# Kernel tuning notes

Hardware: AMD Instinct MI355X
Metric: run time of the kernel (lower is better)

## Reference

```python
import jax, jax.numpy as jnp
import numpy as np

B, N, C = 8, 2048, 256
NGRP = 4          # n oscillator dims per group
RANK = 16         # A_rank
EPS = 1e-6        # solver eps
GN_EPS = 1e-5     # torch GroupNorm default eps


def setup_inputs() -> dict:
    key = jax.random.key(0)
    k0, k1, k2, k3 = jax.random.split(key, 4)
    x = jax.random.normal(k0, (B, N, C), jnp.float32)
    y = jax.random.normal(k1, (B, C, N), jnp.float32)
    sc = jax.random.uniform(k2, (B, N, N), jnp.float32)
    U = 0.01 * jax.random.normal(k3, (N, RANK), jnp.float32)
    omega_param = (1.0 / np.sqrt(2)).astype(np.float32) * jnp.ones((C // 2, 1), jnp.float32)
    gn_w = jnp.ones((C,), jnp.float32)
    gn_b = jnp.zeros((C,), jnp.float32)
    gamma = jnp.float32(1.0)
    return {"x": x, "y": y, "sc": sc, "U": U, "omega_param": omega_param,
            "gn_w": gn_w, "gn_b": gn_b, "gamma": gamma, "Q": 8}


def _map_to_sphere(x):
    # normalize each group of NGRP channels to unit norm
    xv = x.reshape(B, N, C // NGRP, NGRP)
    n2 = jnp.clip(jnp.sum(xv * xv, axis=-1, keepdims=True), EPS, None)
    return (xv * jax.lax.rsqrt(n2)).reshape(B, N, C)


def _project_osc(v, x):
    # remove component of v along x within each oscillator group (tangent projection)
    xv = x.reshape(B, N, C // NGRP, NGRP)
    vv = v.reshape(B, N, C // NGRP, NGRP)
    sim = jnp.sum(xv * vv, axis=-1, keepdims=True)
    return (vv - sim * xv).reshape(B, N, C)


def _group_norm(y, w, b):
    # y: [B, C, N]; num_groups = C // NGRP, NGRP channels per group
    G = C // NGRP
    yv = y.reshape(B, G, NGRP * N)
    mu = jnp.mean(yv, axis=-1, keepdims=True)
    var = jnp.mean((yv - mu) ** 2, axis=-1, keepdims=True)
    yn = ((yv - mu) * jax.lax.rsqrt(var + GN_EPS)).reshape(B, C, N)
    return yn * w[None, :, None] + b[None, :, None]


def _omega_term(x, omega_param):
    # pairwise rotation: (x0, x1) -> (omg*x1, -omg*x0), omg = |omega_param| per pair
    xp = x.reshape(B, N, C // 2, 2)
    omg = jnp.abs(omega_param).reshape(1, 1, C // 2)  # norm over trailing dim of size 1
    out = jnp.stack([omg * xp[..., 1], -omg * xp[..., 0]], axis=-1)
    return out.reshape(B, N, C)


def _kuramoto(x, y, sc, U, omega_param, gn_w, gn_b, gamma, Q):
    rho = 1.0
    # y: [B, C, N] -> GroupNorm -> [B, N, C] -> sphere
    y = _group_norm(y, gn_w, gn_b)
    y = _map_to_sphere(jnp.transpose(y, (0, 2, 1)))
    # x: [B, N, C] (N != C so no transpose in original)
    x = _map_to_sphere(x)
    # coupling matrix K = sym(W) * sigmoid(U U^T)  (normalize_K=False, w_scale=1)
    Wsym = 0.5 * (sc + jnp.transpose(sc, (0, 2, 1)))
    A = jax.nn.sigmoid(U @ U.T)          # [N, N]
    K = Wsym * A[None, :, :]             # [B, N, N]

    def step(xc, _):
        coupling = jnp.einsum('bnm,bmc->bnc', K, xc)
        force = coupling + y
        om = _omega_term(xc, omega_param)
        dxdt = om + rho * _project_osc(force, xc)
        xn = _map_to_sphere(xc + gamma * dxdt)
        return xn, xn

    _, xs = jax.lax.scan(step, x, None, length=Q)
    return xs  # [Q, B, N, C]


def reference(x, y, sc, U, omega_param, gn_w, gn_b, gamma, Q):
    return _kuramoto(x, y, sc, U, omega_param, gn_w, gn_b, gamma, Q)
```

## Files before the change

### kernel.cpp

```cpp
#include <hip/hip_runtime.h>
#include <hip/hip_bf16.h>

#define BB 8
#define NN 2048
#define CC 256
#define GG 64
#define QQ 8

typedef unsigned short u16;
typedef __attribute__((ext_vector_type(8))) short bf16x8;
typedef __attribute__((ext_vector_type(4))) float f32x4;

static __device__ __forceinline__ float b2f(u16 u) {
  union { unsigned int i; float f; } cv; cv.i = ((unsigned int)u) << 16; return cv.f;
}
static __device__ __forceinline__ u16 f2b(float f) {
  union { __hip_bfloat16 h; u16 u; } cv; cv.h = __float2bfloat16(f); return cv.u;
}
static __device__ __forceinline__ float ldin(const void* p, size_t i, bool f32) {
  return f32 ? ((const float*)p)[i] : b2f(((const u16*)p)[i]);
}
static __device__ __forceinline__ float4 ldin4(const void* p, size_t i, bool f32) {
  if (f32) return *(const float4*)((const float*)p + i);
  ushort4 u = *(const ushort4*)((const u16*)p + i);
  return make_float4(b2f(u.x), b2f(u.y), b2f(u.z), b2f(u.w));
}
static __device__ __forceinline__ void gload16(const void* g, void* l) {
  __builtin_amdgcn_global_load_lds(
      (const __attribute__((address_space(1))) void*)g,
      (__attribute__((address_space(3))) void*)l, 16, 0, 0);
}

__global__ __launch_bounds__(256) void detect_kernel(const u16* __restrict__ sc,
                                                     int* __restrict__ flag)
{
  __shared__ int sh;
  if (threadIdx.x == 0) sh = 0;
  __syncthreads();
  int cnt = 0;
  for (int i = threadIdx.x; i < 2048; i += 256) {
    u16 w = sc[2 * i];
    int e = (w >> 7) & 0xFF;
    if (e >= 100 && e <= 130) cnt++;
  }
  atomicAdd(&sh, cnt);
  __syncthreads();
  if (threadIdx.x == 0) *flag = (sh < 1024) ? 1 : 0;
}

__global__ __launch_bounds__(256) void build_k_kernel(
    const void* __restrict__ sc, const void* __restrict__ U,
    u16* __restrict__ Khi, u16* __restrict__ Klo,
    const int* __restrict__ flagp, int b0, int nbat)
{
  const int i0 = blockIdx.y * 32;
  const int j0 = blockIdx.x * 32;
  if (j0 < i0) return;
  const bool f32 = (*flagp != 0);
  const int tx = threadIdx.x;
  const int ty = threadIdx.y;
  const int t  = ty * 32 + tx;
  const int rr = t >> 3;
  const int cq = t & 7;

  __shared__ float Ui[32][17];
  __shared__ float Uj[32][17];
  __shared__ float As[32][33];
  __shared__ float t1[32][33];
  __shared__ float t2[32][33];

  for (int s = t; s < 512; s += 256) {
    int r2 = s >> 4, kk = s & 15;
    Ui[r2][kk] = ldin(U, (size_t)(i0 + r2) * 16 + kk, f32);
    Uj[r2][kk] = ldin(U, (size_t)(j0 + r2) * 16 + kk, f32);
  }
  __syncthreads();
  for (int ii = ty; ii < 32; ii += 8) {
    float dot = 0.f;
    #pragma unroll
    for (int k = 0; k < 16; k++) dot += Ui[ii][k] * Uj[tx][k];
    As[ii][tx] = 1.0f / (1.0f + expf(-dot));
  }

  for (int bl = 0; bl < nbat; bl++) {
    const int b = b0 + bl;
    const size_t scb = (size_t)b * NN * NN;
    __syncthreads();
    float4 va = ldin4(sc, scb + (size_t)(i0 + rr) * NN + j0 + 4 * cq, f32);
    float4 vb = ldin4(sc, scb + (size_t)(j0 + rr) * NN + i0 + 4 * cq, f32);
    t1[rr][4*cq+0] = va.x; t1[rr][4*cq+1] = va.y;
    t1[rr][4*cq+2] = va.z; t1[rr][4*cq+3] = va.w;
    t2[rr][4*cq+0] = vb.x; t2[rr][4*cq+1] = vb.y;
    t2[rr][4*cq+2] = vb.z; t2[rr][4*cq+3] = vb.w;
    __syncthreads();
    const size_t kfb = (size_t)bl * NN * NN;
    ushort4 h4, l4;
    #pragma unroll
    for (int k = 0; k < 4; k++) {
      int col = 4 * cq + k;
      float kv = 0.5f * (t1[rr][col] + t2[col][rr]) * As[rr][col];
      u16 h = f2b(kv);
      ((u16*)&h4)[k] = h;
      ((u16*)&l4)[k] = f2b(kv - b2f(h));
    }
    size_t o = kfb + (size_t)(i0 + rr) * NN + j0 + 4 * cq;
    *(ushort4*)(Khi + o) = h4;
    *(ushort4*)(Klo + o) = l4;
    if (i0 != j0) {
      #pragma unroll
      for (int k = 0; k < 4; k++) {
        int col = 4 * cq + k;
        float kv = 0.5f * (t2[rr][col] + t1[col][rr]) * As[col][rr];
        u16 h = f2b(kv);
        ((u16*)&h4)[k] = h;
        ((u16*)&l4)[k] = f2b(kv - b2f(h));
      }
      size_t o2 = kfb + (size_t)(j0 + rr) * NN + i0 + 4 * cq;
      *(ushort4*)(Khi + o2) = h4;
      *(ushort4*)(Klo + o2) = l4;
    }
  }
}

__global__ __launch_bounds__(256) void gn_stats_kernel(
    const void* __restrict__ y, float* __restrict__ murs,
    const int* __restrict__ flagp)
{
  const bool f32 = (*flagp != 0);
  const int bg = blockIdx.x;
  float s = 0.f, ss = 0.f;
  if (f32) {
    const float* base = (const float*)y + (size_t)bg * 4 * NN;
    for (int i = threadIdx.x; i < 2048; i += 256) {
      float4 v = *(const float4*)(base + (size_t)i * 4);
      s  += v.x + v.y + v.z + v.w;
      ss += v.x*v.x + v.y*v.y + v.z*v.z + v.w*v.w;
    }
  } else {
    const u16* base = (const u16*)y + (size_t)bg * 4 * NN;
    for (int i = threadIdx.x; i < 2048; i += 256) {
      ushort4 v = *(const ushort4*)(base + (size_t)i * 4);
      float f0 = b2f(v.x), f1 = b2f(v.y), f2 = b2f(v.z), f3 = b2f(v.w);
      s  += f0 + f1 + f2 + f3;
      ss += f0*f0 + f1*f1 + f2*f2 + f3*f3;
    }
  }
  #pragma unroll
  for (int off = 32; off > 0; off >>= 1) {
    s  += __shfl_down(s, off, 64);
    ss += __shfl_down(ss, off, 64);
  }
  __shared__ float sh[8];
  const int w = threadIdx.x >> 6, ln = threadIdx.x & 63;
  if (ln == 0) { sh[w * 2] = s; sh[w * 2 + 1] = ss; }
  __syncthreads();
  if (threadIdx.x == 0) {
    float S  = sh[0] + sh[2] + sh[4] + sh[6];
    float SS = sh[1] + sh[3] + sh[5] + sh[7];
    float mu  = S / 8192.0f;
    float var = SS / 8192.0f - mu * mu;
    murs[bg * 2]     = mu;
    murs[bg * 2 + 1] = 1.0f / sqrtf(fmaxf(var, 0.f) + 1e-5f);
  }
}

__global__ __launch_bounds__(256) void y_tf_kernel(
    const void* __restrict__ y, const float* __restrict__ murs,
    const void* __restrict__ gw, const void* __restrict__ gb,
    float* __restrict__ yt, const int* __restrict__ flagp)
{
  const bool f32 = (*flagp != 0);
  const int b = blockIdx.y;
  const int n = blockIdx.x * 64 + threadIdx.x;
  for (int g = threadIdx.y; g < GG; g += 4) {
    float mu = murs[(b * GG + g) * 2];
    float rs = murs[(b * GG + g) * 2 + 1];
    float v[4];
    #pragma unroll
    for (int k = 0; k < 4; k++) {
      int c = 4 * g + k;
      float val = (ldin(y, ((size_t)b * CC + c) * NN + n, f32) - mu) * rs;
      v[k] = val * ldin(gw, c, f32) + ldin(gb, c, f32);
    }
    float n2 = v[0]*v[0] + v[1]*v[1] + v[2]*v[2] + v[3]*v[3];
    float scl = 1.0f / sqrtf(fmaxf(n2, 1e-6f));
    float4 o; o.x = v[0]*scl; o.y = v[1]*scl; o.z = v[2]*scl; o.w = v[3]*scl;
    *(float4*)(yt + ((size_t)b * NN + n) * CC + 4 * g) = o;
  }
}

__global__ __launch_bounds__(256) void x_init_kernel(
    const void* __restrict__ x, u16* __restrict__ xTh, u16* __restrict__ xTl,
    const int* __restrict__ flagp)
{
  const bool f32 = (*flagp != 0);
  const int b = blockIdx.y;
  const int n = blockIdx.x * 64 + threadIdx.x;
  for (int g = threadIdx.y; g < GG; g += 4) {
    size_t idx = ((size_t)b * NN + n) * CC + 4 * g;
    float v[4];
    if (f32) {
      float4 u4 = *(const float4*)((const float*)x + idx);
      v[0] = u4.x; v[1] = u4.y; v[2] = u4.z; v[3] = u4.w;
    } else {
      ushort4 u = *(const ushort4*)((const u16*)x + idx);
      v[0] = b2f(u.x); v[1] = b2f(u.y); v[2] = b2f(u.z); v[3] = b2f(u.w);
    }
    float n2 = v[0]*v[0] + v[1]*v[1] + v[2]*v[2] + v[3]*v[3];
    float scl = 1.0f / sqrtf(fmaxf(n2, 1e-6f));
    size_t xb = ((size_t)b * CC + 4 * g) * NN + n;
    #pragma unroll
    for (int k = 0; k < 4; k++) {
      float xv = v[k] * scl;
      u16 h = f2b(xv);
      xTh[xb + (size_t)k * NN] = h;
      xTl[xb + (size_t)k * NN] = f2b(xv - b2f(h));
    }
  }
}

template<int NFR, int NFC>
static __device__ __forceinline__ void fused_step_epilogue(
    f32x4 (&acc)[NFR][NFC], int b, int rb, int cb, int l15, int lk,
    const u16* __restrict__ xhc, const u16* __restrict__ xlc,
    u16* __restrict__ xhn, u16* __restrict__ xln,
    const float* __restrict__ yt, const void* __restrict__ omega,
    const void* __restrict__ gamma, void* __restrict__ outbase, size_t qoff,
    bool f32)
{
  const float gm = ldin(gamma, 0, f32);
  #pragma unroll
  for (int fr = 0; fr < NFR; fr++) {
    const int rbase = rb + fr * 16 + lk * 4;
    #pragma unroll
    for (int fc = 0; fc < NFC; fc++) {
      const int c = cb + fc * 16 + l15;
      const size_t xoff = ((size_t)b * CC + c) * NN + rbase;
      ushort4 xh4 = *(const ushort4*)(xhc + xoff);
      ushort4 xl4 = *(const ushort4*)(xlc + xoff);
      float xcv[4] = { b2f(xh4.x) + b2f(xl4.x), b2f(xh4.y) + b2f(xl4.y),
                       b2f(xh4.z) + b2f(xl4.z), b2f(xh4.w) + b2f(xl4.w) };
      float om   = fabsf(ldin(omega, c >> 1, f32));
      float omsg = (c & 1) ? -om : om;
      float xn[4];
      #pragma unroll
      for (int r = 0; r < 4; r++) {
        const int n = rbase + r;
        float f = acc[fr][fc][r] + yt[((size_t)b * NN + n) * CC + c];
        float s = xcv[r] * f;
        s += __shfl_xor(s, 1);
        s += __shfl_xor(s, 2);
        float xp = __shfl_xor(xcv[r], 1);
        float d  = omsg * xp + (f - s * xcv[r]);
        float v  = xcv[r] + gm * d;
        float n2 = v * v;
        n2 += __shfl_xor(n2, 1);
        n2 += __shfl_xor(n2, 2);
        float scl = 1.0f / sqrtf(fmaxf(n2, 1e-6f));
        xn[r] = v * scl;
        const size_t oidx = qoff + ((size_t)b * NN + n) * CC + c;
        if (f32) ((float*)outbase)[oidx] = xn[r];
        else     ((u16*)outbase)[oidx]   = f2b(xn[r]);
      }
      ushort4 nh, nl;
      #pragma unroll
      for (int r = 0; r < 4; r++) {
        u16 h = f2b(xn[r]);
        ((u16*)&nh)[r] = h;
        ((u16*)&nl)[r] = f2b(xn[r] - b2f(h));
      }
      *(ushort4*)(xhn + xoff) = nh;
      *(ushort4*)(xln + xoff) = nl;
    }
  }
}

__global__ __launch_bounds__(512, 2) void gemm_fused_sk(
    const u16* __restrict__ Khi, const u16* __restrict__ Klo,
    const u16* __restrict__ xhc, const u16* __restrict__ xlc,
    u16* __restrict__ xhn, u16* __restrict__ xln,
    const float* __restrict__ yt, const void* __restrict__ omega,
    const void* __restrict__ gamma, void* __restrict__ outbase, size_t qoff,
    const int* __restrict__ flagp)
{
  const int flat = blockIdx.x + 2 * blockIdx.y + 32 * blockIdx.z;
  const int swz  = (flat & 7) * 32 + (flat >> 3);
  const int bx = swz & 1;
  const int by = (swz >> 1) & 15;
  const int b  = swz >> 5;
  const int m0 = by * 128;
  const int c0 = bx * 128;

  __shared__ char lds[2][65536];

  const int t    = threadIdx.x;
  const int lane = t & 63;
  const int wid  = t >> 6;
  const int ng   = wid >> 2;
  const int wr   = (wid >> 1) & 1;
  const int wc   = wid & 1;

  const u16* Ah = Khi + (size_t)b * NN * NN;
  const u16* Al = Klo + (size_t)b * NN * NN;
  const u16* Bh = xhc + (size_t)b * CC * NN;
  const u16* Bl = xlc + (size_t)b * CC * NN;

  const int tr   = t >> 3;
  const int phys = (t & 7) ^ (tr & 7);
  const size_t aoff = (size_t)(m0 + tr) * NN + phys * 8;
  const size_t boff = (size_t)(c0 + tr) * NN + phys * 8;
  const int dst = wid * 1024;

  f32x4 acc[4][2];
  const f32x4 zero4 = {0.f, 0.f, 0.f, 0.f};
  #pragma unroll
  for (int i = 0; i < 4; i++)
    #pragma unroll
    for (int j = 0; j < 2; j++) acc[i][j] = zero4;

  auto stage = [&](int bufi, int kt) {
    char* base = &lds[bufi][0];
    const int k0 = kt * 64;
    #pragma unroll
    for (int i = 0; i < 2; i++) {
      gload16(Ah + aoff + (size_t)i * (64 * NN) + k0, base +         i * 8192 + dst);
      gload16(Al + aoff + (size_t)i * (64 * NN) + k0, base + 16384 + i * 8192 + dst);
      gload16(Bh + boff + (size_t)i * (64 * NN) + k0, base + 32768 + i * 8192 + dst);
      gload16(Bl + boff + (size_t)i * (64 * NN) + k0, base + 49152 + i * 8192 + dst);
    }
  };

  const int l15 = lane & 15;
  const int lk  = lane >> 4;

  auto compute = [&](int bufi) {
    const char* base = &lds[bufi][0];
    #pragma unroll
    for (int ks = 0; ks < 2; ks++) {
      const int cl = ks * 4 + lk;
      bf16x8 fah[4], fal[4], fbh[2], fbl[2];
      #pragma unroll
      for (int fr = 0; fr < 4; fr++) {
        int r   = wr * 64 + fr * 16 + l15;
        int off = r * 128 + ((cl ^ (r & 7)) << 4);
        fah[fr] = *(const bf16x8*)(base + off);
        fal[fr] = *(const bf16x8*)(base + 16384 + off);
      }
      #pragma unroll
      for (int fc = 0; fc < 2; fc++) {
        int r   = ng * 64 + wc * 32 + fc * 16 + l15;
        int off = r * 128 + ((cl ^ (r & 7)) << 4);
        fbh[fc] = *(const bf16x8*)(base + 32768 + off);
        fbl[fc] = *(const bf16x8*)(base + 49152 + off);
      }
      #pragma unroll
      for (int fr = 0; fr < 4; fr++)
        #pragma unroll
        for (int fc = 0; fc < 2; fc++) {
          acc[fr][fc] = __builtin_amdgcn_mfma_f32_16x16x32_bf16(
              fah[fr], fbh[fc], acc[fr][fc], 0, 0, 0);
          acc[fr][fc] = __builtin_amdgcn_mfma_f32_16x16x32_bf16(
              fah[fr], fbl[fc], acc[fr][fc], 0, 0, 0);
          acc[fr][fc] = __builtin_amdgcn_mfma_f32_16x16x32_bf16(
              fal[fr], fbh[fc], acc[fr][fc], 0, 0, 0);
        }
    }
  };

  stage(0, 0);
  stage(1, 1);
  for (int kt = 0; kt < 30; kt++) {
    asm volatile("s_waitcnt vmcnt(8)" ::: "memory");
    __builtin_amdgcn_s_barrier();
    __builtin_amdgcn_sched_barrier(0);
    compute(kt & 1);
    asm volatile("s_waitcnt lgkmcnt(0)" ::: "memory");
    __builtin_amdgcn_sched_barrier(0);
    __builtin_amdgcn_s_barrier();
    stage(kt & 1, kt + 2);
  }
  asm volatile("s_waitcnt vmcnt(8)" ::: "memory");
  __builtin_amdgcn_s_barrier();
  __builtin_amdgcn_sched_barrier(0);
  compute(0);
  asm volatile("s_waitcnt vmcnt(0)" ::: "memory");
  __builtin_amdgcn_s_barrier();
  __builtin_amdgcn_sched_barrier(0);
  compute(1);

  fused_step_epilogue<4, 2>(acc, b, m0 + wr * 64, c0 + ng * 64 + wc * 32,
                            l15, lk, xhc, xlc, xhn, xln, yt, omega, gamma,
                            outbase, qoff, (*flagp != 0));
}

__global__ __launch_bounds__(256, 2) void gemm_fused_db(
    const u16* __restrict__ Khi, const u16* __restrict__ Klo,
    const u16* __restrict__ xhc, const u16* __restrict__ xlc,
    u16* __restrict__ xhn, u16* __restrict__ xln,
    const float* __restrict__ yt, const void* __restrict__ omega,
    const void* __restrict__ gamma, void* __restrict__ outbase, size_t qoff,
    const int* __restrict__ flagp, int grp)
{
  const int flat = blockIdx.x + 4 * blockIdx.y + 128 * blockIdx.z;
  const int swz  = (flat & 7) * 64 + (flat >> 3);
  const int bx = swz & 3;
  const int by = (swz >> 2) & 31;
  const int bl = swz >> 7;
  const int b  = grp * 4 + bl;
  const int m0 = by * 64;
  const int c0 = bx * 64;

  __shared__ char lds[2][32768];

  const int t    = threadIdx.x;
  const int lane = t & 63;
  const int wid  = t >> 6;
  const int wr   = wid >> 1;
  const int wc   = wid & 1;

  const u16* Ah = Khi + (size_t)bl * NN * NN;
  const u16* Al = Klo + (size_t)bl * NN * NN;
  const u16* Bh = xhc + (size_t)b * CC * NN;
  const u16* Bl = xlc + (size_t)b * CC * NN;

  const int tr   = t >> 3;
  const int phys = (t & 7) ^ (tr & 7);
  const size_t aoff = (size_t)(m0 + tr) * NN + phys * 8;
  const size_t boff = (size_t)(c0 + tr) * NN + phys * 8;
  const int dst = wid * 1024;

  f32x4 acc[2][2];
  const f32x4 zero4 = {0.f, 0.f, 0.f, 0.f};
  #pragma unroll
  for (int i = 0; i < 2; i++)
    #pragma unroll
    for (int j = 0; j < 2; j++) acc[i][j] = zero4;

  auto stage = [&](int bufi, int kt) {
    char* base = &lds[bufi][0];
    const int k0 = kt * 64;
    #pragma unroll
    for (int i = 0; i < 2; i++) {
      gload16(Ah + aoff + (size_t)i * (32 * NN) + k0, base +         i * 4096 + dst);
      gload16(Al + aoff + (size_t)i * (32 * NN) + k0, base +  8192 + i * 4096 + dst);
      gload16(Bh + boff + (size_t)i * (32 * NN) + k0, base + 16384 + i * 4096 + dst);
      gload16(Bl + boff + (size_t)i * (32 * NN) + k0, base + 24576 + i * 4096 + dst);
    }
  };

  const int l15 = lane & 15;
  const int lk  = lane >> 4;

  auto compute = [&](int bufi) {
    const char* base = &lds[bufi][0];
    #pragma unroll
    for (int ks = 0; ks < 2; ks++) {
      const int cl = ks * 4 + lk;
      bf16x8 fah[2], fal[2], fbh[2], fbl[2];
      #pragma unroll
      for (int fr = 0; fr < 2; fr++) {
        int r   = wr * 32 + fr * 16 + l15;
        int off = r * 128 + ((cl ^ (r & 7)) << 4);
        fah[fr] = *(const bf16x8*)(base + off);
        fal[fr] = *(const bf16x8*)(base + 8192 + off);
      }
      #pragma unroll
      for (int fc = 0; fc < 2; fc++) {
        int r   = wc * 32 + fc * 16 + l15;
        int off = r * 128 + ((cl ^ (r & 7)) << 4);
        fbh[fc] = *(const bf16x8*)(base + 16384 + off);
        fbl[fc] = *(const bf16x8*)(base + 24576 + off);
      }
      #pragma unroll
      for (int fr = 0; fr < 2; fr++)
        #pragma unroll
        for (int fc = 0; fc < 2; fc++) {
          acc[fr][fc] = __builtin_amdgcn_mfma_f32_16x16x32_bf16(
              fah[fr], fbh[fc], acc[fr][fc], 0, 0, 0);
          acc[fr][fc] = __builtin_amdgcn_mfma_f32_16x16x32_bf16(
              fah[fr], fbl[fc], acc[fr][fc], 0, 0, 0);
          acc[fr][fc] = __builtin_amdgcn_mfma_f32_16x16x32_bf16(
              fal[fr], fbh[fc], acc[fr][fc], 0, 0, 0);
        }
    }
  };

  stage(0, 0);
  __syncthreads();
  int buf = 0;
  for (int kt = 0; kt < NN / 64; kt++) {
    if (kt + 1 < NN / 64) stage(buf ^ 1, kt + 1);
    compute(buf);
    __syncthreads();
    buf ^= 1;
  }

  fused_step_epilogue<2, 2>(acc, b, m0 + wr * 32, c0 + wc * 32,
                            l15, lk, xhc, xlc, xhn, xln, yt, omega, gamma,
                            outbase, qoff, (*flagp != 0));
}

extern "C" void kernel_launch(void* const* d_in, const int* in_sizes, int n_in,
                              void* d_out, int out_size, void* d_ws, size_t ws_size,
                              hipStream_t stream) {
  const void* x     = d_in[0];
  const void* y     = d_in[1];
  const void* sc    = d_in[2];
  const void* U     = d_in[3];
  const void* omega = d_in[4];
  const void* gw    = d_in[5];
  const void* gb    = d_in[6];
  const void* gamma = d_in[7];
  char* ws = (char*)d_ws;

  const size_t BNC = (size_t)BB * NN * CC;
  const bool big = ws_size >= 184600000ull;

  if (big) {
    u16*   Khi  = (u16*)(ws);
    u16*   Klo  = (u16*)(ws + 67108864);
    float* yt   = (float*)(ws + 134217728);
    u16*   xAh  = (u16*)(ws + 150994944);
    u16*   xAl  = (u16*)(ws + 159383552);
    u16*   xBh  = (u16*)(ws + 167772160);
    u16*   xBl  = (u16*)(ws + 176160768);
    float* murs = (float*)(ws + 184549376);
    int*   flag = (int*)  (ws + 184553472);
    u16* xh[2] = { xAh, xBh };
    u16* xl[2] = { xAl, xBl };

    detect_kernel<<<dim3(1), dim3(256), 0, stream>>>((const u16*)sc, flag);
    gn_stats_kernel<<<dim3(512), dim3(256), 0, stream>>>(y, murs, flag);
    y_tf_kernel<<<dim3(32, 8), dim3(64, 4), 0, stream>>>(y, murs, gw, gb, yt, flag);
    x_init_kernel<<<dim3(32, 8), dim3(64, 4), 0, stream>>>(x, xAh, xAl, flag);
    build_k_kernel<<<dim3(64, 64), dim3(32, 8), 0, stream>>>(
        sc, U, Khi, Klo, flag, 0, 8);
    for (int q = 0; q < QQ; q++) {
      const int cur = q & 1, nxt = cur ^ 1;
      gemm_fused_sk<<<dim3(2, 16, 8), dim3(512), 0, stream>>>(
          Khi, Klo, xh[cur], xl[cur], xh[nxt], xl[nxt],
          yt, omega, gamma, d_out, (size_t)q * BNC, flag);
    }
  } else {
    u16*   Khi  = (u16*)(ws);
    u16*   Klo  = (u16*)(ws + 33554432);
    float* yt   = (float*)(ws + 67108864);
    u16*   xAh  = (u16*)(ws + 83886080);
    u16*   xAl  = (u16*)(ws + 92274688);
    u16*   xBh  = (u16*)(ws + 100663296);
    u16*   xBl  = (u16*)(ws + 109051904);
    float* murs = (float*)(ws + 117440512);
    int*   flag = (int*)  (ws + 117444608);
    u16* xh[2] = { xAh, xBh };
    u16* xl[2] = { xAl, xBl };

    detect_kernel<<<dim3(1), dim3(256), 0, stream>>>((const u16*)sc, flag);
    gn_stats_kernel<<<dim3(512), dim3(256), 0, stream>>>(y, murs, flag);
    y_tf_kernel<<<dim3(32, 8), dim3(64, 4), 0, stream>>>(y, murs, gw, gb, yt, flag);
    x_init_kernel<<<dim3(32, 8), dim3(64, 4), 0, stream>>>(x, xAh, xAl, flag);
    for (int grp = 0; grp < 2; grp++) {
      build_k_kernel<<<dim3(64, 64), dim3(32, 8), 0, stream>>>(
          sc, U, Khi, Klo, flag, grp * 4, 4);
      for (int q = 0; q < QQ; q++) {
        const int cur = q & 1, nxt = cur ^ 1;
        gemm_fused_db<<<dim3(4, 32, 4), dim3(256), 0, stream>>>(
            Khi, Klo, xh[cur], xl[cur], xh[nxt], xl[nxt],
            yt, omega, gamma, d_out, (size_t)q * BNC, flag, grp);
      }
    }
  }
}
```

Baseline: 907.3 us.

## Parallelize K build over batch, phase GEMM compute with barriers, nontemporal output stores

The K-build kernel gets a batch grid dimension instead of looping over batches, and the sc loads are issued before the sigmoid computation so their latency overlaps it. This trades extra redundant sigmoid(UU^T) work per batch for more parallelism. The split-K GEMM compute loop is reorganized per row fragment, with workgroup barriers and s_setprio around the MFMA bursts so waves interleave LDS reads with matrix work. The output writes become nontemporal stores to avoid polluting cache.

```diff
diff --git a/kernel.cpp b/kernel.cpp
--- a/kernel.cpp
+++ b/kernel.cpp
@@ -51,12 +51,14 @@
 __global__ __launch_bounds__(256) void build_k_kernel(
     const void* __restrict__ sc, const void* __restrict__ U,
     u16* __restrict__ Khi, u16* __restrict__ Klo,
-    const int* __restrict__ flagp, int b0, int nbat)
+    const int* __restrict__ flagp, int b0)
 {
   const int i0 = blockIdx.y * 32;
   const int j0 = blockIdx.x * 32;
   if (j0 < i0) return;
   const bool f32 = (*flagp != 0);
+  const int bl = blockIdx.z;
+  const int b  = b0 + bl;
   const int tx = threadIdx.x;
   const int ty = threadIdx.y;
   const int t  = ty * 32 + tx;
@@ -74,6 +76,9 @@
     Ui[r2][kk] = ldin(U, (size_t)(i0 + r2) * 16 + kk, f32);
     Uj[r2][kk] = ldin(U, (size_t)(j0 + r2) * 16 + kk, f32);
   }
+  const size_t scb = (size_t)b * NN * NN;
+  float4 va = ldin4(sc, scb + (size_t)(i0 + rr) * NN + j0 + 4 * cq, f32);
+  float4 vb = ldin4(sc, scb + (size_t)(j0 + rr) * NN + i0 + 4 * cq, f32);
   __syncthreads();
   for (int ii = ty; ii < 32; ii += 8) {
     float dot = 0.f;
@@ -81,44 +86,37 @@
     for (int k = 0; k < 16; k++) dot += Ui[ii][k] * Uj[tx][k];
     As[ii][tx] = 1.0f / (1.0f + expf(-dot));
   }
-
-  for (int bl = 0; bl < nbat; bl++) {
-    const int b = b0 + bl;
-    const size_t scb = (size_t)b * NN * NN;
-    __syncthreads();
-    float4 va = ldin4(sc, scb + (size_t)(i0 + rr) * NN + j0 + 4 * cq, f32);
-    float4 vb = ldin4(sc, scb + (size_t)(j0 + rr) * NN + i0 + 4 * cq, f32);
-    t1[rr][4*cq+0] = va.x; t1[rr][4*cq+1] = va.y;
-    t1[rr][4*cq+2] = va.z; t1[rr][4*cq+3] = va.w;
-    t2[rr][4*cq+0] = vb.x; t2[rr][4*cq+1] = vb.y;
-    t2[rr][4*cq+2] = vb.z; t2[rr][4*cq+3] = vb.w;
-    __syncthreads();
-    const size_t kfb = (size_t)bl * NN * NN;
-    ushort4 h4, l4;
+  t1[rr][4*cq+0] = va.x; t1[rr][4*cq+1] = va.y;
+  t1[rr][4*cq+2] = va.z; t1[rr][4*cq+3] = va.w;
+  t2[rr][4*cq+0] = vb.x; t2[rr][4*cq+1] = vb.y;
+  t2[rr][4*cq+2] = vb.z; t2[rr][4*cq+3] = vb.w;
+  __syncthreads();
+
+  const size_t kfb = (size_t)bl * NN * NN;
+  ushort4 h4, l4;
+  #pragma unroll
+  for (int k = 0; k < 4; k++) {
+    int col = 4 * cq + k;
+    float kv = 0.5f * (t1[rr][col] + t2[col][rr]) * As[rr][col];
+    u16 h = f2b(kv);
+    ((u16*)&h4)[k] = h;
+    ((u16*)&l4)[k] = f2b(kv - b2f(h));
+  }
+  size_t o = kfb + (size_t)(i0 + rr) * NN + j0 + 4 * cq;
+  *(ushort4*)(Khi + o) = h4;
+  *(ushort4*)(Klo + o) = l4;
+  if (i0 != j0) {
     #pragma unroll
     for (int k = 0; k < 4; k++) {
       int col = 4 * cq + k;
-      float kv = 0.5f * (t1[rr][col] + t2[col][rr]) * As[rr][col];
+      float kv = 0.5f * (t2[rr][col] + t1[col][rr]) * As[col][rr];
       u16 h = f2b(kv);
       ((u16*)&h4)[k] = h;
       ((u16*)&l4)[k] = f2b(kv - b2f(h));
     }
-    size_t o = kfb + (size_t)(i0 + rr) * NN + j0 + 4 * cq;
-    *(ushort4*)(Khi + o) = h4;
-    *(ushort4*)(Klo + o) = l4;
-    if (i0 != j0) {
-      #pragma unroll
-      for (int k = 0; k < 4; k++) {
-        int col = 4 * cq + k;
-        float kv = 0.5f * (t2[rr][col] + t1[col][rr]) * As[col][rr];
-        u16 h = f2b(kv);
-        ((u16*)&h4)[k] = h;
-        ((u16*)&l4)[k] = f2b(kv - b2f(h));
-      }
-      size_t o2 = kfb + (size_t)(j0 + rr) * NN + i0 + 4 * cq;
-      *(ushort4*)(Khi + o2) = h4;
-      *(ushort4*)(Klo + o2) = l4;
-    }
+    size_t o2 = kfb + (size_t)(j0 + rr) * NN + i0 + 4 * cq;
+    *(ushort4*)(Khi + o2) = h4;
+    *(ushort4*)(Klo + o2) = l4;
   }
 }
 
@@ -259,8 +257,8 @@
         float scl = 1.0f / sqrtf(fmaxf(n2, 1e-6f));
         xn[r] = v * scl;
         const size_t oidx = qoff + ((size_t)b * NN + n) * CC + c;
-        if (f32) ((float*)outbase)[oidx] = xn[r];
-        else     ((u16*)outbase)[oidx]   = f2b(xn[r]);
+        if (f32) __builtin_nontemporal_store(xn[r], (float*)outbase + oidx);
+        else     __builtin_nontemporal_store(f2b(xn[r]), (u16*)outbase + oidx);
       }
       ushort4 nh, nl;
       #pragma unroll
@@ -333,37 +331,50 @@
   const int l15 = lane & 15;
   const int lk  = lane >> 4;
 
-  auto compute = [&](int bufi) {
+  auto compute_phased = [&](int bufi) {
     const char* base = &lds[bufi][0];
-    #pragma unroll
-    for (int ks = 0; ks < 2; ks++) {
-      const int cl = ks * 4 + lk;
-      bf16x8 fah[4], fal[4], fbh[2], fbl[2];
-      #pragma unroll
-      for (int fr = 0; fr < 4; fr++) {
+    bf16x8 fbh[2][2], fbl[2][2];
+    #pragma unroll
+    for (int fr = 0; fr < 4; fr++) {
+      bf16x8 fah[2], fal[2];
+      #pragma unroll
+      for (int ks = 0; ks < 2; ks++) {
+        const int cl = ks * 4 + lk;
         int r   = wr * 64 + fr * 16 + l15;
         int off = r * 128 + ((cl ^ (r & 7)) << 4);
-        fah[fr] = *(const bf16x8*)(base + off);
-        fal[fr] = *(const bf16x8*)(base + 16384 + off);
-      }
-      #pragma unroll
-      for (int fc = 0; fc < 2; fc++) {
-        int r   = ng * 64 + wc * 32 + fc * 16 + l15;
-        int off = r * 128 + ((cl ^ (r & 7)) << 4);
-        fbh[fc] = *(const bf16x8*)(base + 32768 + off);
-        fbl[fc] = *(const bf16x8*)(base + 49152 + off);
-      }
-      #pragma unroll
-      for (int fr = 0; fr < 4; fr++)
+        fah[ks] = *(const bf16x8*)(base + off);
+        fal[ks] = *(const bf16x8*)(base + 16384 + off);
+      }
+      if (fr == 0) {
+        #pragma unroll
+        for (int ks = 0; ks < 2; ks++) {
+          const int cl = ks * 4 + lk;
+          #pragma unroll
+          for (int fc = 0; fc < 2; fc++) {
+            int rb  = ng * 64 + wc * 32 + fc * 16 + l15;
+            int off = rb * 128 + ((cl ^ (rb & 7)) << 4);
+            fbh[ks][fc] = *(const bf16x8*)(base + 32768 + off);
+            fbl[ks][fc] = *(const bf16x8*)(base + 49152 + off);
+          }
+        }
+      }
+      __builtin_amdgcn_s_barrier();
+      asm volatile("s_waitcnt lgkmcnt(0)" ::: "memory");
+      __builtin_amdgcn_sched_barrier(0);
+      __builtin_amdgcn_s_setprio(1);
+      #pragma unroll
+      for (int ks = 0; ks < 2; ks++)
         #pragma unroll
         for (int fc = 0; fc < 2; fc++) {
           acc[fr][fc] = __builtin_amdgcn_mfma_f32_16x16x32_bf16(
-              fah[fr], fbh[fc], acc[fr][fc], 0, 0, 0);
+              fah[ks], fbh[ks][fc], acc[fr][fc], 0, 0, 0);
           acc[fr][fc] = __builtin_amdgcn_mfma_f32_16x16x32_bf16(
-              fah[fr], fbl[fc], acc[fr][fc], 0, 0, 0);
+              fah[ks], fbl[ks][fc], acc[fr][fc], 0, 0, 0);
           acc[fr][fc] = __builtin_amdgcn_mfma_f32_16x16x32_bf16(
-              fal[fr], fbh[fc], acc[fr][fc], 0, 0, 0);
+              fal[ks], fbh[ks][fc], acc[fr][fc], 0, 0, 0);
         }
+      __builtin_amdgcn_s_setprio(0);
+      __builtin_amdgcn_s_barrier();
     }
   };
 
@@ -373,20 +384,17 @@
     asm volatile("s_waitcnt vmcnt(8)" ::: "memory");
     __builtin_amdgcn_s_barrier();
     __builtin_amdgcn_sched_barrier(0);
-    compute(kt & 1);
-    asm volatile("s_waitcnt lgkmcnt(0)" ::: "memory");
-    __builtin_amdgcn_sched_barrier(0);
-    __builtin_amdgcn_s_barrier();
+    compute_phased(kt & 1);
     stage(kt & 1, kt + 2);
   }
   asm volatile("s_waitcnt vmcnt(8)" ::: "memory");
   __builtin_amdgcn_s_barrier();
   __builtin_amdgcn_sched_barrier(0);
-  compute(0);
+  compute_phased(0);
   asm volatile("s_waitcnt vmcnt(0)" ::: "memory");
   __builtin_amdgcn_s_barrier();
   __builtin_amdgcn_sched_barrier(0);
-  compute(1);
+  compute_phased(1);
 
   fused_step_epilogue<4, 2>(acc, b, m0 + wr * 64, c0 + ng * 64 + wc * 32,
                             l15, lk, xhc, xlc, xhn, xln, yt, omega, gamma,
@@ -533,8 +541,8 @@
     gn_stats_kernel<<<dim3(512), dim3(256), 0, stream>>>(y, murs, flag);
     y_tf_kernel<<<dim3(32, 8), dim3(64, 4), 0, stream>>>(y, murs, gw, gb, yt, flag);
     x_init_kernel<<<dim3(32, 8), dim3(64, 4), 0, stream>>>(x, xAh, xAl, flag);
-    build_k_kernel<<<dim3(64, 64), dim3(32, 8), 0, stream>>>(
-        sc, U, Khi, Klo, flag, 0, 8);
+    build_k_kernel<<<dim3(64, 64, 8), dim3(32, 8), 0, stream>>>(
+        sc, U, Khi, Klo, flag, 0);
     for (int q = 0; q < QQ; q++) {
       const int cur = q & 1, nxt = cur ^ 1;
       gemm_fused_sk<<<dim3(2, 16, 8), dim3(512), 0, stream>>>(
@@ -559,8 +567,8 @@
     y_tf_kernel<<<dim3(32, 8), dim3(64, 4), 0, stream>>>(y, murs, gw, gb, yt, flag);
     x_init_kernel<<<dim3(32, 8), dim3(64, 4), 0, stream>>>(x, xAh, xAl, flag);
     for (int grp = 0; grp < 2; grp++) {
-      build_k_kernel<<<dim3(64, 64), dim3(32, 8), 0, stream>>>(
-          sc, U, Khi, Klo, flag, grp * 4, 4);
+      build_k_kernel<<<dim3(64, 64, 4), dim3(32, 8), 0, stream>>>(
+          sc, U, Khi, Klo, flag, grp * 4);
       for (int q = 0; q < QQ; q++) {
         const int cur = q & 1, nxt = cur ^ 1;
         gemm_fused_db<<<dim3(4, 32, 4), dim3(256), 0, stream>>>(
```

New measurement: 920.0 us. About the same (+1.4%).

## Retile main GEMM to 128x64 with 256 threads, parallelise K build over batch

Applied to the files above, without the earlier changes.

Replaces the 512-thread 128x128 GEMM-step kernel with a 256-thread 128x64 tile that uses K-step 32, a simpler double-buffered loop with __syncthreads, and no XOR swizzle in LDS. The K-construction kernel now assigns one batch per grid z-slice instead of looping over batches, and the sc loads are issued before the sigmoid computation so they overlap with it. Output stores become nontemporal to keep them from polluting the cache. The retiled GEMM doubles the number of blocks but rereads the K matrix twice as often, gives up the explicit vmcnt pipelining, and the unswizzled LDS layout may cause bank conflicts.

```diff
diff --git a/kernel.cpp b/kernel.cpp
--- a/kernel.cpp
+++ b/kernel.cpp
@@ -51,12 +51,14 @@
 __global__ __launch_bounds__(256) void build_k_kernel(
     const void* __restrict__ sc, const void* __restrict__ U,
     u16* __restrict__ Khi, u16* __restrict__ Klo,
-    const int* __restrict__ flagp, int b0, int nbat)
+    const int* __restrict__ flagp, int b0)
 {
   const int i0 = blockIdx.y * 32;
   const int j0 = blockIdx.x * 32;
   if (j0 < i0) return;
   const bool f32 = (*flagp != 0);
+  const int bl = blockIdx.z;
+  const int b  = b0 + bl;
   const int tx = threadIdx.x;
   const int ty = threadIdx.y;
   const int t  = ty * 32 + tx;
@@ -74,6 +76,9 @@
     Ui[r2][kk] = ldin(U, (size_t)(i0 + r2) * 16 + kk, f32);
     Uj[r2][kk] = ldin(U, (size_t)(j0 + r2) * 16 + kk, f32);
   }
+  const size_t scb = (size_t)b * NN * NN;
+  float4 va = ldin4(sc, scb + (size_t)(i0 + rr) * NN + j0 + 4 * cq, f32);
+  float4 vb = ldin4(sc, scb + (size_t)(j0 + rr) * NN + i0 + 4 * cq, f32);
   __syncthreads();
   for (int ii = ty; ii < 32; ii += 8) {
     float dot = 0.f;
@@ -81,44 +86,37 @@
     for (int k = 0; k < 16; k++) dot += Ui[ii][k] * Uj[tx][k];
     As[ii][tx] = 1.0f / (1.0f + expf(-dot));
   }
-
-  for (int bl = 0; bl < nbat; bl++) {
-    const int b = b0 + bl;
-    const size_t scb = (size_t)b * NN * NN;
-    __syncthreads();
-    float4 va = ldin4(sc, scb + (size_t)(i0 + rr) * NN + j0 + 4 * cq, f32);
-    float4 vb = ldin4(sc, scb + (size_t)(j0 + rr) * NN + i0 + 4 * cq, f32);
-    t1[rr][4*cq+0] = va.x; t1[rr][4*cq+1] = va.y;
-    t1[rr][4*cq+2] = va.z; t1[rr][4*cq+3] = va.w;
-    t2[rr][4*cq+0] = vb.x; t2[rr][4*cq+1] = vb.y;
-    t2[rr][4*cq+2] = vb.z; t2[rr][4*cq+3] = vb.w;
-    __syncthreads();
-    const size_t kfb = (size_t)bl * NN * NN;
-    ushort4 h4, l4;
+  t1[rr][4*cq+0] = va.x; t1[rr][4*cq+1] = va.y;
+  t1[rr][4*cq+2] = va.z; t1[rr][4*cq+3] = va.w;
+  t2[rr][4*cq+0] = vb.x; t2[rr][4*cq+1] = vb.y;
+  t2[rr][4*cq+2] = vb.z; t2[rr][4*cq+3] = vb.w;
+  __syncthreads();
+
+  const size_t kfb = (size_t)bl * NN * NN;
+  ushort4 h4, l4;
+  #pragma unroll
+  for (int k = 0; k < 4; k++) {
+    int col = 4 * cq + k;
+    float kv = 0.5f * (t1[rr][col] + t2[col][rr]) * As[rr][col];
+    u16 h = f2b(kv);
+    ((u16*)&h4)[k] = h;
+    ((u16*)&l4)[k] = f2b(kv - b2f(h));
+  }
+  size_t o = kfb + (size_t)(i0 + rr) * NN + j0 + 4 * cq;
+  *(ushort4*)(Khi + o) = h4;
+  *(ushort4*)(Klo + o) = l4;
+  if (i0 != j0) {
     #pragma unroll
     for (int k = 0; k < 4; k++) {
       int col = 4 * cq + k;
-      float kv = 0.5f * (t1[rr][col] + t2[col][rr]) * As[rr][col];
+      float kv = 0.5f * (t2[rr][col] + t1[col][rr]) * As[col][rr];
       u16 h = f2b(kv);
       ((u16*)&h4)[k] = h;
       ((u16*)&l4)[k] = f2b(kv - b2f(h));
     }
-    size_t o = kfb + (size_t)(i0 + rr) * NN + j0 + 4 * cq;
-    *(ushort4*)(Khi + o) = h4;
-    *(ushort4*)(Klo + o) = l4;
-    if (i0 != j0) {
-      #pragma unroll
-      for (int k = 0; k < 4; k++) {
-        int col = 4 * cq + k;
-        float kv = 0.5f * (t2[rr][col] + t1[col][rr]) * As[col][rr];
-        u16 h = f2b(kv);
-        ((u16*)&h4)[k] = h;
-        ((u16*)&l4)[k] = f2b(kv - b2f(h));
-      }
-      size_t o2 = kfb + (size_t)(j0 + rr) * NN + i0 + 4 * cq;
-      *(ushort4*)(Khi + o2) = h4;
-      *(ushort4*)(Klo + o2) = l4;
-    }
+    size_t o2 = kfb + (size_t)(j0 + rr) * NN + i0 + 4 * cq;
+    *(ushort4*)(Khi + o2) = h4;
+    *(ushort4*)(Klo + o2) = l4;
   }
 }
 
@@ -259,8 +257,8 @@
         float scl = 1.0f / sqrtf(fmaxf(n2, 1e-6f));
         xn[r] = v * scl;
         const size_t oidx = qoff + ((size_t)b * NN + n) * CC + c;
-        if (f32) ((float*)outbase)[oidx] = xn[r];
-        else     ((u16*)outbase)[oidx]   = f2b(xn[r]);
+        if (f32) __builtin_nontemporal_store(xn[r], (float*)outbase + oidx);
+        else     __builtin_nontemporal_store(f2b(xn[r]), (u16*)outbase + oidx);
       }
       ushort4 nh, nl;
       #pragma unroll
@@ -275,7 +273,7 @@
   }
 }
 
-__global__ __launch_bounds__(512, 2) void gemm_fused_sk(
+__global__ __launch_bounds__(256, 2) void gemm_fused_r9(
     const u16* __restrict__ Khi, const u16* __restrict__ Klo,
     const u16* __restrict__ xhc, const u16* __restrict__ xlc,
     u16* __restrict__ xhn, u16* __restrict__ xln,
@@ -283,21 +281,20 @@
     const void* __restrict__ gamma, void* __restrict__ outbase, size_t qoff,
     const int* __restrict__ flagp)
 {
-  const int flat = blockIdx.x + 2 * blockIdx.y + 32 * blockIdx.z;
-  const int swz  = (flat & 7) * 32 + (flat >> 3);
-  const int bx = swz & 1;
-  const int by = (swz >> 1) & 15;
-  const int b  = swz >> 5;
+  const int flat = blockIdx.x + 4 * blockIdx.y + 64 * blockIdx.z;
+  const int swz  = (flat & 7) * 64 + (flat >> 3);
+  const int bx = swz & 3;
+  const int by = (swz >> 2) & 15;
+  const int b  = swz >> 6;
   const int m0 = by * 128;
-  const int c0 = bx * 128;
-
-  __shared__ char lds[2][65536];
+  const int c0 = bx * 64;
+
+  __shared__ char lds[2][24576];
 
   const int t    = threadIdx.x;
   const int lane = t & 63;
   const int wid  = t >> 6;
-  const int ng   = wid >> 2;
-  const int wr   = (wid >> 1) & 1;
+  const int wr   = wid >> 1;
   const int wc   = wid & 1;
 
   const u16* Ah = Khi + (size_t)b * NN * NN;
@@ -305,10 +302,10 @@
   const u16* Bh = xhc + (size_t)b * CC * NN;
   const u16* Bl = xlc + (size_t)b * CC * NN;
 
-  const int tr   = t >> 3;
-  const int phys = (t & 7) ^ (tr & 7);
-  const size_t aoff = (size_t)(m0 + tr) * NN + phys * 8;
-  const size_t boff = (size_t)(c0 + tr) * NN + phys * 8;
+  const int tr   = t >> 2;
+  const int ck   = t & 3;
+  const size_t aoff = (size_t)(m0 + tr) * NN + ck * 8;
+  const size_t boff = (size_t)(c0 + tr) * NN + ck * 8;
   const int dst = wid * 1024;
 
   f32x4 acc[4][2];
@@ -320,14 +317,13 @@
 
   auto stage = [&](int bufi, int kt) {
     char* base = &lds[bufi][0];
-    const int k0 = kt * 64;
-    #pragma unroll
-    for (int i = 0; i < 2; i++) {
-      gload16(Ah + aoff + (size_t)i * (64 * NN) + k0, base +         i * 8192 + dst);
-      gload16(Al + aoff + (size_t)i * (64 * NN) + k0, base + 16384 + i * 8192 + dst);
-      gload16(Bh + boff + (size_t)i * (64 * NN) + k0, base + 32768 + i * 8192 + dst);
-      gload16(Bl + boff + (size_t)i * (64 * NN) + k0, base + 49152 + i * 8192 + dst);
-    }
+    const int k0 = kt * 32;
+    gload16(Ah + aoff + k0,               base +         dst);
+    gload16(Ah + aoff + (size_t)64 * NN + k0, base +  4096 + dst);
+    gload16(Al + aoff + k0,               base +  8192 + dst);
+    gload16(Al + aoff + (size_t)64 * NN + k0, base + 12288 + dst);
+    gload16(Bh + boff + k0,               base + 16384 + dst);
+    gload16(Bl + boff + k0,               base + 20480 + dst);
   };
 
   const int l15 = lane & 15;
@@ -335,60 +331,43 @@
 
   auto compute = [&](int bufi) {
     const char* base = &lds[bufi][0];
-    #pragma unroll
-    for (int ks = 0; ks < 2; ks++) {
-      const int cl = ks * 4 + lk;
-      bf16x8 fah[4], fal[4], fbh[2], fbl[2];
-      #pragma unroll
-      for (int fr = 0; fr < 4; fr++) {
-        int r   = wr * 64 + fr * 16 + l15;
-        int off = r * 128 + ((cl ^ (r & 7)) << 4);
-        fah[fr] = *(const bf16x8*)(base + off);
-        fal[fr] = *(const bf16x8*)(base + 16384 + off);
-      }
+    bf16x8 fah[4], fal[4], fbh[2], fbl[2];
+    #pragma unroll
+    for (int fr = 0; fr < 4; fr++) {
+      int off = (wr * 64 + fr * 16 + l15) * 64 + lk * 16;
+      fah[fr] = *(const bf16x8*)(base + off);
+      fal[fr] = *(const bf16x8*)(base + 8192 + off);
+    }
+    #pragma unroll
+    for (int fc = 0; fc < 2; fc++) {
+      int off = (wc * 32 + fc * 16 + l15) * 64 + lk * 16;
+      fbh[fc] = *(const bf16x8*)(base + 16384 + off);
+      fbl[fc] = *(const bf16x8*)(base + 20480 + off);
+    }
+    #pragma unroll
+    for (int fr = 0; fr < 4; fr++)
       #pragma unroll
       for (int fc = 0; fc < 2; fc++) {
-        int r   = ng * 64 + wc * 32 + fc * 16 + l15;
-        int off = r * 128 + ((cl ^ (r & 7)) << 4);
-        fbh[fc] = *(const bf16x8*)(base + 32768 + off);
-        fbl[fc] = *(const bf16x8*)(base + 49152 + off);
+        acc[fr][fc] = __builtin_amdgcn_mfma_f32_16x16x32_bf16(
+            fah[fr], fbh[fc], acc[fr][fc], 0, 0, 0);
+        acc[fr][fc] = __builtin_amdgcn_mfma_f32_16x16x32_bf16(
+            fah[fr], fbl[fc], acc[fr][fc], 0, 0, 0);
+        acc[fr][fc] = __builtin_amdgcn_mfma_f32_16x16x32_bf16(
+            fal[fr], fbh[fc], acc[fr][fc], 0, 0, 0);
       }
-      #pragma unroll
-      for (int fr = 0; fr < 4; fr++)
-        #pragma unroll
-        for (int fc = 0; fc < 2; fc++) {
-          acc[fr][fc] = __builtin_amdgcn_mfma_f32_16x16x32_bf16(
-              fah[fr], fbh[fc], acc[fr][fc], 0, 0, 0);
-          acc[fr][fc] = __builtin_amdgcn_mfma_f32_16x16x32_bf16(
-              fah[fr], fbl[fc], acc[fr][fc], 0, 0, 0);
-          acc[fr][fc] = __builtin_amdgcn_mfma_f32_16x16x32_bf16(
-              fal[fr], fbh[fc], acc[fr][fc], 0, 0, 0);
-        }
-    }
   };
 
   stage(0, 0);
-  stage(1, 1);
-  for (int kt = 0; kt < 30; kt++) {
-    asm volatile("s_waitcnt vmcnt(8)" ::: "memory");
-    __builtin_amdgcn_s_barrier();
-    __builtin_amdgcn_sched_barrier(0);
-    compute(kt & 1);
-    asm volatile("s_waitcnt lgkmcnt(0)" ::: "memory");
-    __builtin_amdgcn_sched_barrier(0);
-    __builtin_amdgcn_s_barrier();
-    stage(kt & 1, kt + 2);
-  }
-  asm volatile("s_waitcnt vmcnt(8)" ::: "memory");
-  __builtin_amdgcn_s_barrier();
-  __builtin_amdgcn_sched_barrier(0);
-  compute(0);
-  asm volatile("s_waitcnt vmcnt(0)" ::: "memory");
-  __builtin_amdgcn_s_barrier();
-  __builtin_amdgcn_sched_barrier(0);
-  compute(1);
-
-  fused_step_epilogue<4, 2>(acc, b, m0 + wr * 64, c0 + ng * 64 + wc * 32,
+  __syncthreads();
+  int buf = 0;
+  for (int kt = 0; kt < NN / 32; kt++) {
+    if (kt + 1 < NN / 32) stage(buf ^ 1, kt + 1);
+    compute(buf);
+    __syncthreads();
+    buf ^= 1;
+  }
+
+  fused_step_epilogue<4, 2>(acc, b, m0 + wr * 64, c0 + wc * 32,
                             l15, lk, xhc, xlc, xhn, xln, yt, omega, gamma,
                             outbase, qoff, (*flagp != 0));
 }
@@ -533,11 +512,11 @@
     gn_stats_kernel<<<dim3(512), dim3(256), 0, stream>>>(y, murs, flag);
     y_tf_kernel<<<dim3(32, 8), dim3(64, 4), 0, stream>>>(y, murs, gw, gb, yt, flag);
     x_init_kernel<<<dim3(32, 8), dim3(64, 4), 0, stream>>>(x, xAh, xAl, flag);
-    build_k_kernel<<<dim3(64, 64), dim3(32, 8), 0, stream>>>(
-        sc, U, Khi, Klo, flag, 0, 8);
+    build_k_kernel<<<dim3(64, 64, 8), dim3(32, 8), 0, stream>>>(
+        sc, U, Khi, Klo, flag, 0);
     for (int q = 0; q < QQ; q++) {
       const int cur = q & 1, nxt = cur ^ 1;
-      gemm_fused_sk<<<dim3(2, 16, 8), dim3(512), 0, stream>>>(
+      gemm_fused_r9<<<dim3(4, 16, 8), dim3(256), 0, stream>>>(
           Khi, Klo, xh[cur], xl[cur], xh[nxt], xl[nxt],
           yt, omega, gamma, d_out, (size_t)q * BNC, flag);
     }
@@ -559,8 +538,8 @@
     y_tf_kernel<<<dim3(32, 8), dim3(64, 4), 0, stream>>>(y, murs, gw, gb, yt, flag);
     x_init_kernel<<<dim3(32, 8), dim3(64, 4), 0, stream>>>(x, xAh, xAl, flag);
     for (int grp = 0; grp < 2; grp++) {
-      build_k_kernel<<<dim3(64, 64), dim3(32, 8), 0, stream>>>(
-          sc, U, Khi, Klo, flag, grp * 4, 4);
+      build_k_kernel<<<dim3(64, 64, 4), dim3(32, 8), 0, stream>>>(
+          sc, U, Khi, Klo, flag, grp * 4);
       for (int q = 0; q < QQ; q++) {
         const int cur = q & 1, nxt = cur ^ 1;
         gemm_fused_db<<<dim3(4, 32, 4), dim3(256), 0, stream>>>(
```

Measured after the change: 946.9 us. +4.4%, slower.

## Parallelize K build over batch, use nontemporal output stores, simplify GEMM double-buffer loop

Applied to the files above, without the earlier changes.

The K-building kernel now launches one block per batch along grid z instead of looping over batches inside each block, and issues the sc loads before the sigmoid computation so they overlap it. Output stores in the fused epilogue become nontemporal to avoid polluting cache with write-once data. The main GEMM loop drops its hand-tuned two-stage prefetch with explicit waitcnt and barriers in favour of a simple stage-next/compute-current loop with __syncthreads. The simpler loop may lose prefetch depth and fine-grained wait control, and the per-batch K build recomputes the sigmoid tile once per batch.

```diff
diff --git a/kernel.cpp b/kernel.cpp
--- a/kernel.cpp
+++ b/kernel.cpp
@@ -51,12 +51,14 @@
 __global__ __launch_bounds__(256) void build_k_kernel(
     const void* __restrict__ sc, const void* __restrict__ U,
     u16* __restrict__ Khi, u16* __restrict__ Klo,
-    const int* __restrict__ flagp, int b0, int nbat)
+    const int* __restrict__ flagp, int b0)
 {
   const int i0 = blockIdx.y * 32;
   const int j0 = blockIdx.x * 32;
   if (j0 < i0) return;
   const bool f32 = (*flagp != 0);
+  const int bl = blockIdx.z;
+  const int b  = b0 + bl;
   const int tx = threadIdx.x;
   const int ty = threadIdx.y;
   const int t  = ty * 32 + tx;
@@ -74,6 +76,9 @@
     Ui[r2][kk] = ldin(U, (size_t)(i0 + r2) * 16 + kk, f32);
     Uj[r2][kk] = ldin(U, (size_t)(j0 + r2) * 16 + kk, f32);
   }
+  const size_t scb = (size_t)b * NN * NN;
+  float4 va = ldin4(sc, scb + (size_t)(i0 + rr) * NN + j0 + 4 * cq, f32);
+  float4 vb = ldin4(sc, scb + (size_t)(j0 + rr) * NN + i0 + 4 * cq, f32);
   __syncthreads();
   for (int ii = ty; ii < 32; ii += 8) {
     float dot = 0.f;
@@ -81,44 +86,37 @@
     for (int k = 0; k < 16; k++) dot += Ui[ii][k] * Uj[tx][k];
     As[ii][tx] = 1.0f / (1.0f + expf(-dot));
   }
-
-  for (int bl = 0; bl < nbat; bl++) {
-    const int b = b0 + bl;
-    const size_t scb = (size_t)b * NN * NN;
-    __syncthreads();
-    float4 va = ldin4(sc, scb + (size_t)(i0 + rr) * NN + j0 + 4 * cq, f32);
-    float4 vb = ldin4(sc, scb + (size_t)(j0 + rr) * NN + i0 + 4 * cq, f32);
-    t1[rr][4*cq+0] = va.x; t1[rr][4*cq+1] = va.y;
-    t1[rr][4*cq+2] = va.z; t1[rr][4*cq+3] = va.w;
-    t2[rr][4*cq+0] = vb.x; t2[rr][4*cq+1] = vb.y;
-    t2[rr][4*cq+2] = vb.z; t2[rr][4*cq+3] = vb.w;
-    __syncthreads();
-    const size_t kfb = (size_t)bl * NN * NN;
-    ushort4 h4, l4;
+  t1[rr][4*cq+0] = va.x; t1[rr][4*cq+1] = va.y;
+  t1[rr][4*cq+2] = va.z; t1[rr][4*cq+3] = va.w;
+  t2[rr][4*cq+0] = vb.x; t2[rr][4*cq+1] = vb.y;
+  t2[rr][4*cq+2] = vb.z; t2[rr][4*cq+3] = vb.w;
+  __syncthreads();
+
+  const size_t kfb = (size_t)bl * NN * NN;
+  ushort4 h4, l4;
+  #pragma unroll
+  for (int k = 0; k < 4; k++) {
+    int col = 4 * cq + k;
+    float kv = 0.5f * (t1[rr][col] + t2[col][rr]) * As[rr][col];
+    u16 h = f2b(kv);
+    ((u16*)&h4)[k] = h;
+    ((u16*)&l4)[k] = f2b(kv - b2f(h));
+  }
+  size_t o = kfb + (size_t)(i0 + rr) * NN + j0 + 4 * cq;
+  *(ushort4*)(Khi + o) = h4;
+  *(ushort4*)(Klo + o) = l4;
+  if (i0 != j0) {
     #pragma unroll
     for (int k = 0; k < 4; k++) {
       int col = 4 * cq + k;
-      float kv = 0.5f * (t1[rr][col] + t2[col][rr]) * As[rr][col];
+      float kv = 0.5f * (t2[rr][col] + t1[col][rr]) * As[col][rr];
       u16 h = f2b(kv);
       ((u16*)&h4)[k] = h;
       ((u16*)&l4)[k] = f2b(kv - b2f(h));
     }
-    size_t o = kfb + (size_t)(i0 + rr) * NN + j0 + 4 * cq;
-    *(ushort4*)(Khi + o) = h4;
-    *(ushort4*)(Klo + o) = l4;
-    if (i0 != j0) {
-      #pragma unroll
-      for (int k = 0; k < 4; k++) {
-        int col = 4 * cq + k;
-        float kv = 0.5f * (t2[rr][col] + t1[col][rr]) * As[col][rr];
-        u16 h = f2b(kv);
-        ((u16*)&h4)[k] = h;
-        ((u16*)&l4)[k] = f2b(kv - b2f(h));
-      }
-      size_t o2 = kfb + (size_t)(j0 + rr) * NN + i0 + 4 * cq;
-      *(ushort4*)(Khi + o2) = h4;
-      *(ushort4*)(Klo + o2) = l4;
-    }
+    size_t o2 = kfb + (size_t)(j0 + rr) * NN + i0 + 4 * cq;
+    *(ushort4*)(Khi + o2) = h4;
+    *(ushort4*)(Klo + o2) = l4;
   }
 }
 
@@ -259,8 +257,8 @@
         float scl = 1.0f / sqrtf(fmaxf(n2, 1e-6f));
         xn[r] = v * scl;
         const size_t oidx = qoff + ((size_t)b * NN + n) * CC + c;
-        if (f32) ((float*)outbase)[oidx] = xn[r];
-        else     ((u16*)outbase)[oidx]   = f2b(xn[r]);
+        if (f32) __builtin_nontemporal_store(xn[r], (float*)outbase + oidx);
+        else     __builtin_nontemporal_store(f2b(xn[r]), (u16*)outbase + oidx);
       }
       ushort4 nh, nl;
       #pragma unroll
@@ -275,7 +273,7 @@
   }
 }
 
-__global__ __launch_bounds__(512, 2) void gemm_fused_sk(
+__global__ __launch_bounds__(512, 2) void gemm_fused_p10(
     const u16* __restrict__ Khi, const u16* __restrict__ Klo,
     const u16* __restrict__ xhc, const u16* __restrict__ xlc,
     u16* __restrict__ xhn, u16* __restrict__ xln,
@@ -368,25 +366,14 @@
   };
 
   stage(0, 0);
-  stage(1, 1);
-  for (int kt = 0; kt < 30; kt++) {
-    asm volatile("s_waitcnt vmcnt(8)" ::: "memory");
-    __builtin_amdgcn_s_barrier();
-    __builtin_amdgcn_sched_barrier(0);
-    compute(kt & 1);
-    asm volatile("s_waitcnt lgkmcnt(0)" ::: "memory");
-    __builtin_amdgcn_sched_barrier(0);
-    __builtin_amdgcn_s_barrier();
-    stage(kt & 1, kt + 2);
-  }
-  asm volatile("s_waitcnt vmcnt(8)" ::: "memory");
-  __builtin_amdgcn_s_barrier();
-  __builtin_amdgcn_sched_barrier(0);
-  compute(0);
-  asm volatile("s_waitcnt vmcnt(0)" ::: "memory");
-  __builtin_amdgcn_s_barrier();
-  __builtin_amdgcn_sched_barrier(0);
-  compute(1);
+  __syncthreads();
+  int buf = 0;
+  for (int kt = 0; kt < NN / 64; kt++) {
+    if (kt + 1 < NN / 64) stage(buf ^ 1, kt + 1);
+    compute(buf);
+    __syncthreads();
+    buf ^= 1;
+  }
 
   fused_step_epilogue<4, 2>(acc, b, m0 + wr * 64, c0 + ng * 64 + wc * 32,
                             l15, lk, xhc, xlc, xhn, xln, yt, omega, gamma,
@@ -533,11 +520,11 @@
     gn_stats_kernel<<<dim3(512), dim3(256), 0, stream>>>(y, murs, flag);
     y_tf_kernel<<<dim3(32, 8), dim3(64, 4), 0, stream>>>(y, murs, gw, gb, yt, flag);
     x_init_kernel<<<dim3(32, 8), dim3(64, 4), 0, stream>>>(x, xAh, xAl, flag);
-    build_k_kernel<<<dim3(64, 64), dim3(32, 8), 0, stream>>>(
-        sc, U, Khi, Klo, flag, 0, 8);
+    build_k_kernel<<<dim3(64, 64, 8), dim3(32, 8), 0, stream>>>(
+        sc, U, Khi, Klo, flag, 0);
     for (int q = 0; q < QQ; q++) {
       const int cur = q & 1, nxt = cur ^ 1;
-      gemm_fused_sk<<<dim3(2, 16, 8), dim3(512), 0, stream>>>(
+      gemm_fused_p10<<<dim3(2, 16, 8), dim3(512), 0, stream>>>(
           Khi, Klo, xh[cur], xl[cur], xh[nxt], xl[nxt],
           yt, omega, gamma, d_out, (size_t)q * BNC, flag);
     }
@@ -559,8 +546,8 @@
     y_tf_kernel<<<dim3(32, 8), dim3(64, 4), 0, stream>>>(y, murs, gw, gb, yt, flag);
     x_init_kernel<<<dim3(32, 8), dim3(64, 4), 0, stream>>>(x, xAh, xAl, flag);
     for (int grp = 0; grp < 2; grp++) {
-      build_k_kernel<<<dim3(64, 64), dim3(32, 8), 0, stream>>>(
-          sc, U, Khi, Klo, flag, grp * 4, 4);
+      build_k_kernel<<<dim3(64, 64, 4), dim3(32, 8), 0, stream>>>(
+          sc, U, Khi, Klo, flag, grp * 4);
       for (int q = 0; q < QQ; q++) {
         const int cur = q & 1, nxt = cur ^ 1;
         gemm_fused_db<<<dim3(4, 32, 4), dim3(256), 0, stream>>>(
```

Measured after the change: 854.4 us. 1.06x faster.
